# Optimization experiments

Hardware: AMD Instinct MI355X
Metric: run time of the kernel (lower is better)

The kernel has to match this reference:

```python
import jax, jax.numpy as jnp
import numpy as np

NEG_INF = -1e30  # stand-in for float('-inf') masked_fill (safe for softmax)


def setup_inputs() -> dict:
    key = jax.random.key(0)
    ks = jax.random.split(key, 7)
    B, T, C, H, D = 4, 2048, 64, 6, 64
    s = 1.0 / np.sqrt(C)
    return {
        "x": jax.random.normal(ks[0], (B, T, C), dtype=jnp.float32),
        "y": jax.random.normal(ks[1], (B, T, C), dtype=jnp.float32),
        "Wq": jax.random.normal(ks[2], (H, C, D), dtype=jnp.float32) * s,
        "Wk": jax.random.normal(ks[3], (H, C, D), dtype=jnp.float32) * s,
        "Wv": jax.random.normal(ks[4], (H, C, D), dtype=jnp.float32) * s,
        "W_proj": jax.random.normal(ks[5], (H * D, C), dtype=jnp.float32) * (1.0 / np.sqrt(H * D)),
        "b_proj": jnp.zeros((C,), dtype=jnp.float32),
    }


def reference(x, y, Wq, Wk, Wv, W_proj, b_proj):
    # x, y: [B, T, C]; per-head projections stacked over H (heads vectorized).
    B, T, C = x.shape
    H, _, D = Wq.shape
    q = jnp.einsum("btc,hcd->bhtd", x, Wq)   # query from decoder input x
    k = jnp.einsum("btc,hcd->bhtd", y, Wk)   # key from encoder output y
    v = jnp.einsum("btc,hcd->bhtd", y, Wv)
    scale = D ** (-0.5)
    wei = jnp.einsum("bhtd,bhsd->bhts", q, k) * scale  # [B,H,T,T]
    # triu(ones(T,T), diagonal=1) future mask (causal)
    future = jnp.triu(jnp.ones((T, T), dtype=bool), k=1)
    wei = jnp.where(future, NEG_INF, wei)
    wei = jax.nn.softmax(wei, axis=-1)  # dropout = identity in eval
    out = jnp.einsum("bhts,bhsd->bhtd", wei, v)          # [B,H,T,D]
    out = out.transpose(0, 2, 1, 3).reshape(B, T, H * D)  # concat heads
    return out @ W_proj + b_proj                          # [B,T,C]
```

## Files before the change

### kernel.cpp

```cpp
#include <hip/hip_runtime.h>


typedef unsigned short u16t;
typedef __attribute__((ext_vector_type(8))) short short8;
typedef __attribute__((ext_vector_type(4))) float float4v;

#define MFMA16(a, b, c) __builtin_amdgcn_mfma_f32_16x16x32_bf16((a), (b), (c), 0, 0, 0)

__device__ __forceinline__ float fexp2(float x) {
  return __builtin_amdgcn_exp2f(x);
}
__device__ __forceinline__ float bf2f(u16t u) {
  return __uint_as_float(((unsigned)u) << 16);
}
__device__ __forceinline__ u16t f2bf(float f) {
  unsigned u = __float_as_uint(f);
  u += 0x7fffu + ((u >> 16) & 1u);
  return (u16t)(u >> 16);
}
__device__ __forceinline__ u16t f2bf_trunc(float f) {
  return (u16t)(__float_as_uint(f) >> 16);
}
__device__ __forceinline__ short8 load8_f32_bf16(const float* p) {
  float4 f0 = *(const float4*)p;
  float4 f1 = *(const float4*)(p + 4);
  short8 r;
  r[0] = (short)f2bf(f0.x); r[1] = (short)f2bf(f0.y);
  r[2] = (short)f2bf(f0.z); r[3] = (short)f2bf(f0.w);
  r[4] = (short)f2bf(f1.x); r[5] = (short)f2bf(f1.y);
  r[6] = (short)f2bf(f1.z); r[7] = (short)f2bf(f1.w);
  return r;
}

constexpr int Bb = 4, Tt = 2048, Cc = 64, Hh = 6, Dd = 64;
constexpr int BH = Bb * Hh;
constexpr int NQT = Tt / 64;
constexpr int LDT = 72;
constexpr int LDV = 136;
#define QSCALE (0.125f * 1.44269504088896f)

__global__ __launch_bounds__(256) void qkv_kernel(
    const float* __restrict__ x, const float* __restrict__ y,
    const float* __restrict__ Wq, const float* __restrict__ Wk,
    const float* __restrict__ Wv,
    u16t* __restrict__ Q, u16t* __restrict__ K, u16t* __restrict__ Vt) {
  __shared__ __align__(16) u16t wtq[64 * LDT];
  __shared__ __align__(16) u16t wtk[64 * LDT];
  __shared__ __align__(16) u16t wtv[64 * LDT];

  int bid = blockIdx.x;
  int bh = bid >> 5, tt = bid & 31;
  int b = bh / Hh, h = bh - b * Hh;
  int tid = threadIdx.x;
  int w = tid >> 6, lane = tid & 63;
  int l15 = lane & 15, q4 = lane >> 4;

  {
    const float4* wq4 = (const float4*)(Wq + h * 4096);
    const float4* wk4 = (const float4*)(Wk + h * 4096);
    const float4* wv4 = (const float4*)(Wv + h * 4096);
#pragma unroll
    for (int i = 0; i < 4; ++i) {
      int fidx = tid + i * 256;
      float4 qv = wq4[fidx], kv = wk4[fidx], vv = wv4[fidx];
      int base = fidx * 4;
      int c = base >> 6, d0 = base & 63;
      wtq[(d0 + 0) * LDT + c] = f2bf(qv.x);
      wtq[(d0 + 1) * LDT + c] = f2bf(qv.y);
      wtq[(d0 + 2) * LDT + c] = f2bf(qv.z);
      wtq[(d0 + 3) * LDT + c] = f2bf(qv.w);
      wtk[(d0 + 0) * LDT + c] = f2bf(kv.x);
      wtk[(d0 + 1) * LDT + c] = f2bf(kv.y);
      wtk[(d0 + 2) * LDT + c] = f2bf(kv.z);
      wtk[(d0 + 3) * LDT + c] = f2bf(kv.w);
      wtv[(d0 + 0) * LDT + c] = f2bf(vv.x);
      wtv[(d0 + 1) * LDT + c] = f2bf(vv.y);
      wtv[(d0 + 2) * LDT + c] = f2bf(vv.z);
      wtv[(d0 + 3) * LDT + c] = f2bf(vv.w);
    }
  }

  int trow = tt * 64 + w * 16 + l15;
  const float* xrow = x + ((size_t)b * Tt + trow) * Cc;
  const float* yrow = y + ((size_t)b * Tt + trow) * Cc;
  short8 xa[2], ya[2];
#pragma unroll
  for (int kc = 0; kc < 2; ++kc) {
    xa[kc] = load8_f32_bf16(xrow + kc * 32 + q4 * 8);
    ya[kc] = load8_f32_bf16(yrow + kc * 32 + q4 * 8);
  }
  __syncthreads();

  float4v qa4[4], ka4[4], va4[4];
#pragma unroll
  for (int nc = 0; nc < 4; ++nc) {
    qa4[nc] = (float4v){0.f, 0.f, 0.f, 0.f};
    ka4[nc] = (float4v){0.f, 0.f, 0.f, 0.f};
    va4[nc] = (float4v){0.f, 0.f, 0.f, 0.f};
  }
#pragma unroll
  for (int nc = 0; nc < 4; ++nc) {
#pragma unroll
    for (int kc = 0; kc < 2; ++kc) {
      int off = (nc * 16 + l15) * LDT + kc * 32 + q4 * 8;
      short8 bq = *(const short8*)&wtq[off];
      short8 bk = *(const short8*)&wtk[off];
      short8 bv = *(const short8*)&wtv[off];
      qa4[nc] = MFMA16(xa[kc], bq, qa4[nc]);
      ka4[nc] = MFMA16(ya[kc], bk, ka4[nc]);
      va4[nc] = MFMA16(ya[kc], bv, va4[nc]);
    }
  }
  __syncthreads();

#pragma unroll
  for (int reg = 0; reg < 4; ++reg) {
    int rloc = w * 16 + q4 * 4 + reg;
#pragma unroll
    for (int nc = 0; nc < 4; ++nc) {
      wtq[rloc * LDT + nc * 16 + l15] = f2bf(qa4[nc][reg] * QSCALE);
      wtk[rloc * LDT + nc * 16 + l15] = f2bf(ka4[nc][reg]);
      wtv[(nc * 16 + l15) * LDT + rloc] = f2bf(va4[nc][reg]);
    }
  }
  __syncthreads();

  size_t tilebase = ((size_t)bh * Tt + tt * 64) * Dd;
#pragma unroll
  for (int i = 0; i < 2; ++i) {
    int id = tid * 2 + i;
    int row = id >> 3, c8 = id & 7;
    *(uint4*)&Q[tilebase + row * 64 + c8 * 8] = *(const uint4*)&wtq[row * LDT + c8 * 8];
    *(uint4*)&K[tilebase + row * 64 + c8 * 8] = *(const uint4*)&wtk[row * LDT + c8 * 8];
    *(uint4*)&Vt[((size_t)bh * 64 + row) * Tt + tt * 64 + c8 * 8] =
        *(const uint4*)&wtv[row * LDT + c8 * 8];
  }
}

__global__ __launch_bounds__(256) void attn_kernel(
    const u16t* __restrict__ Q, const u16t* __restrict__ K,
    const u16t* __restrict__ Vt, u16t* __restrict__ att) {
  __shared__ __align__(16) u16t Kl[128 * LDT];
  __shared__ __align__(16) u16t Vl[64 * LDV];
  __shared__ __align__(16) u16t Pl[4 * 16 * LDV];

  int bid = blockIdx.x;
  int bh = bid % BH;
  int qt = (NQT - 1) - bid / BH;
  int b = bh / Hh, h = bh - (bh / Hh) * Hh;
  int tid = threadIdx.x;
  int w = tid >> 6;
  int lane = tid & 63;
  int l15 = lane & 15, q4 = lane >> 4;

  const u16t* Qbase = Q + ((size_t)bh * Tt + qt * 64 + w * 16 + l15) * Dd;
  short8 qf0 = *(const short8*)(Qbase + q4 * 8);
  short8 qf1 = *(const short8*)(Qbase + 32 + q4 * 8);

  float4v O[4];
#pragma unroll
  for (int nc = 0; nc < 4; ++nc) O[nc] = (float4v){0.f, 0.f, 0.f, 0.f};
  float l_[4] = {0.f, 0.f, 0.f, 0.f};

  const u16t* Kbh = K + (size_t)bh * Tt * Dd;
  const u16t* Vbh = Vt + (size_t)bh * Dd * Tt;
  u16t* Pw = Pl + w * 16 * LDV;
  const int jmax = qt >> 1;

  for (int jt = 0; jt <= jmax; ++jt) {
    __syncthreads();
    {
      const u16t* ksrc = Kbh + (size_t)jt * 128 * 64;
      const u16t* vsrc = Vbh + jt * 128;
#pragma unroll
      for (int i = 0; i < 4; ++i) {
        int ci = tid + i * 256;
        int kr = ci >> 3, kc8 = ci & 7;
        *(uint4*)&Kl[kr * LDT + kc8 * 8] = *(const uint4*)(ksrc + kr * 64 + kc8 * 8);
        int vd = ci >> 4, vj8 = ci & 15;
        *(uint4*)&Vl[vd * LDV + vj8 * 8] = *(const uint4*)(vsrc + (size_t)vd * Tt + vj8 * 8);
      }
    }
    __syncthreads();

    float4v S[8];
#pragma unroll
    for (int nc = 0; nc < 8; ++nc) {
      short8 kf0 = *(const short8*)&Kl[(nc * 16 + l15) * LDT + q4 * 8];
      short8 kf1 = *(const short8*)&Kl[(nc * 16 + l15) * LDT + 32 + q4 * 8];
      float4v s = (float4v){0.f, 0.f, 0.f, 0.f};
      s = MFMA16(qf0, kf0, s);
      s = MFMA16(qf1, kf1, s);
      S[nc] = s;
    }

    if (jt == jmax) {
      int rloc = qt * 64 + w * 16 + q4 * 4;
      int cbase = jt * 128 + l15;
#pragma unroll
      for (int nc = 0; nc < 8; ++nc)
#pragma unroll
        for (int reg = 0; reg < 4; ++reg)
          if (cbase + nc * 16 > rloc + reg) S[nc][reg] = -1e30f;
    }

#pragma unroll
    for (int nc = 0; nc < 8; ++nc) {
#pragma unroll
      for (int reg = 0; reg < 4; ++reg) {
        float p = fexp2(S[nc][reg]);
        l_[reg] += p;
        Pw[(q4 * 4 + reg) * LDV + nc * 16 + l15] = f2bf_trunc(p);
      }
    }

    short8 pf[4];
#pragma unroll
    for (int kc2 = 0; kc2 < 4; ++kc2)
      pf[kc2] = *(const short8*)&Pw[l15 * LDV + kc2 * 32 + q4 * 8];
#pragma unroll
    for (int nc = 0; nc < 4; ++nc) {
#pragma unroll
      for (int kc2 = 0; kc2 < 4; ++kc2) {
        short8 vf = *(const short8*)&Vl[(nc * 16 + l15) * LDV + kc2 * 32 + q4 * 8];
        O[nc] = MFMA16(pf[kc2], vf, O[nc]);
      }
    }
  }

#pragma unroll
  for (int reg = 0; reg < 4; ++reg) {
    float s = l_[reg];
#pragma unroll
    for (int off = 1; off < 16; off <<= 1) s += __shfl_xor(s, off);
    float inv = 1.0f / s;
    int t = qt * 64 + w * 16 + q4 * 4 + reg;
    size_t obase = ((size_t)b * Tt + t) * (Hh * Dd) + h * Dd;
#pragma unroll
    for (int nc = 0; nc < 4; ++nc)
      att[obase + nc * 16 + l15] = f2bf(O[nc][reg] * inv);
  }
}

constexpr int LDP = 392;

__global__ __launch_bounds__(256) void proj_kernel(
    const u16t* __restrict__ att, const float* __restrict__ Wp,
    const float* __restrict__ bp, float* __restrict__ out) {
  __shared__ __align__(16) u16t wpt[64 * LDP];

  int bid = blockIdx.x;
  int tid = threadIdx.x;
  int w = tid >> 6, lane = tid & 63;
  int l15 = lane & 15, q4 = lane >> 4;

  const float4* wp4 = (const float4*)Wp;
#pragma unroll
  for (int i = 0; i < 24; ++i) {
    int fidx = tid + i * 256;
    float4 v = wp4[fidx];
    int base = fidx * 4;
    int r = base >> 6, c0 = base & 63;
    wpt[(c0 + 0) * LDP + r] = f2bf(v.x);
    wpt[(c0 + 1) * LDP + r] = f2bf(v.y);
    wpt[(c0 + 2) * LDP + r] = f2bf(v.z);
    wpt[(c0 + 3) * LDP + r] = f2bf(v.w);
  }
  __syncthreads();

  int row0 = bid * 64 + w * 16;
  const u16t* arow = att + (size_t)(row0 + l15) * 384;

  float4v acc[4];
#pragma unroll
  for (int nc = 0; nc < 4; ++nc) acc[nc] = (float4v){0.f, 0.f, 0.f, 0.f};

#pragma unroll
  for (int kc = 0; kc < 12; ++kc) {
    short8 a = *(const short8*)(arow + kc * 32 + q4 * 8);
#pragma unroll
    for (int nc = 0; nc < 4; ++nc) {
      short8 bfr = *(const short8*)&wpt[(nc * 16 + l15) * LDP + kc * 32 + q4 * 8];
      acc[nc] = MFMA16(a, bfr, acc[nc]);
    }
  }

  float bv[4];
#pragma unroll
  for (int nc = 0; nc < 4; ++nc) bv[nc] = bp[nc * 16 + l15];
#pragma unroll
  for (int reg = 0; reg < 4; ++reg) {
    int t = row0 + q4 * 4 + reg;
    size_t obase = (size_t)t * 64;
#pragma unroll
    for (int nc = 0; nc < 4; ++nc)
      out[obase + nc * 16 + l15] = acc[nc][reg] + bv[nc];
  }
}

extern "C" void kernel_launch(void* const* d_in, const int* in_sizes, int n_in,
                              void* d_out, int out_size, void* d_ws, size_t ws_size,
                              hipStream_t stream) {
  const float* x  = (const float*)d_in[0];
  const float* y  = (const float*)d_in[1];
  const float* Wq = (const float*)d_in[2];
  const float* Wk = (const float*)d_in[3];
  const float* Wv = (const float*)d_in[4];
  const float* Wp = (const float*)d_in[5];
  const float* bp = (const float*)d_in[6];
  float* out = (float*)d_out;

  const size_t NBH = (size_t)BH * Tt * Dd;
  u16t* Qs   = (u16t*)d_ws;
  u16t* Ks   = Qs + NBH;
  u16t* Vts  = Ks + NBH;
  u16t* attb = Vts + NBH;

  qkv_kernel<<<BH * NQT, 256, 0, stream>>>(x, y, Wq, Wk, Wv, Qs, Ks, Vts);
  attn_kernel<<<BH * NQT, 256, 0, stream>>>(Qs, Ks, Vts, attb);
  proj_kernel<<<(Bb * Tt) / 64, 256, 0, stream>>>(attb, Wp, bp, out);
}
```

Measured before the change: 122.5 us.

## Restructure attention to split key tiles across waves and reduce outputs in LDS

The attention kernel now gives each wave 16 keys of a 64-key tile for all 64 query rows, instead of one 16-row query slice against 128 keys. Scores are computed transposed so the probabilities feed the PV MFMA straight from registers, which removes the P round-trip through shared memory. The cost is that half of each 32-wide MFMA K dimension is zero-padded, and partial O and row sums must be reduced across waves through LDS. Shared memory shrinks and launch bounds request 3 blocks per CU to raise occupancy, while each thread now holds 16 accumulator vectors, which raises register pressure.

```diff
diff --git a/kernel.cpp b/kernel.cpp
--- a/kernel.cpp
+++ b/kernel.cpp
@@ -6,6 +6,8 @@
 typedef __attribute__((ext_vector_type(4))) float float4v;
 
 #define MFMA16(a, b, c) __builtin_amdgcn_mfma_f32_16x16x32_bf16((a), (b), (c), 0, 0, 0)
+
+union U8 { short8 s; unsigned u[4]; };
 
 __device__ __forceinline__ float fexp2(float x) {
   return __builtin_amdgcn_exp2f(x);
@@ -18,8 +20,8 @@
   u += 0x7fffu + ((u >> 16) & 1u);
   return (u16t)(u >> 16);
 }
-__device__ __forceinline__ u16t f2bf_trunc(float f) {
-  return (u16t)(__float_as_uint(f) >> 16);
+__device__ __forceinline__ unsigned bftr(float f) {
+  return __float_as_uint(f) >> 16;
 }
 __device__ __forceinline__ short8 load8_f32_bf16(const float* p) {
   float4 f0 = *(const float4*)p;
@@ -36,7 +38,7 @@
 constexpr int BH = Bb * Hh;
 constexpr int NQT = Tt / 64;
 constexpr int LDT = 72;
-constexpr int LDV = 136;
+constexpr int OST = 65;
 #define QSCALE (0.125f * 1.44269504088896f)
 
 __global__ __launch_bounds__(256) void qkv_kernel(
@@ -137,12 +139,14 @@
   }
 }
 
-__global__ __launch_bounds__(256) void attn_kernel(
+__global__ __launch_bounds__(256, 3) void attn_kernel(
     const u16t* __restrict__ Q, const u16t* __restrict__ K,
     const u16t* __restrict__ Vt, u16t* __restrict__ att) {
-  __shared__ __align__(16) u16t Kl[128 * LDT];
-  __shared__ __align__(16) u16t Vl[64 * LDV];
-  __shared__ __align__(16) u16t Pl[4 * 16 * LDV];
+  __shared__ __align__(16) unsigned char smem[64 * LDT * 2 * 2 + 256];
+  u16t* Kl = (u16t*)smem;
+  u16t* Vl = (u16t*)(smem + 64 * LDT * 2);
+  float* Ol = (float*)smem;
+  float* Ll = (float*)(smem + 64 * LDT * 2 * 2);
 
   int bid = blockIdx.x;
   int bh = bid % BH;
@@ -153,92 +157,110 @@
   int lane = tid & 63;
   int l15 = lane & 15, q4 = lane >> 4;
 
-  const u16t* Qbase = Q + ((size_t)bh * Tt + qt * 64 + w * 16 + l15) * Dd;
-  short8 qf0 = *(const short8*)(Qbase + q4 * 8);
-  short8 qf1 = *(const short8*)(Qbase + 32 + q4 * 8);
-
-  float4v O[4];
-#pragma unroll
-  for (int nc = 0; nc < 4; ++nc) O[nc] = (float4v){0.f, 0.f, 0.f, 0.f};
+  short8 qf[4][2];
+#pragma unroll
+  for (int it = 0; it < 4; ++it) {
+    const u16t* qb = Q + ((size_t)bh * Tt + qt * 64 + it * 16 + l15) * Dd;
+    qf[it][0] = *(const short8*)(qb + q4 * 8);
+    qf[it][1] = *(const short8*)(qb + 32 + q4 * 8);
+  }
+
+  float4v O[4][4];
+#pragma unroll
+  for (int it = 0; it < 4; ++it)
+#pragma unroll
+    for (int nc = 0; nc < 4; ++nc) O[it][nc] = (float4v){0.f, 0.f, 0.f, 0.f};
   float l_[4] = {0.f, 0.f, 0.f, 0.f};
 
   const u16t* Kbh = K + (size_t)bh * Tt * Dd;
   const u16t* Vbh = Vt + (size_t)bh * Dd * Tt;
-  u16t* Pw = Pl + w * 16 * LDV;
-  const int jmax = qt >> 1;
-
-  for (int jt = 0; jt <= jmax; ++jt) {
+
+  for (int jt = 0; jt <= qt; ++jt) {
     __syncthreads();
     {
-      const u16t* ksrc = Kbh + (size_t)jt * 128 * 64;
-      const u16t* vsrc = Vbh + jt * 128;
-#pragma unroll
-      for (int i = 0; i < 4; ++i) {
-        int ci = tid + i * 256;
-        int kr = ci >> 3, kc8 = ci & 7;
-        *(uint4*)&Kl[kr * LDT + kc8 * 8] = *(const uint4*)(ksrc + kr * 64 + kc8 * 8);
-        int vd = ci >> 4, vj8 = ci & 15;
-        *(uint4*)&Vl[vd * LDV + vj8 * 8] = *(const uint4*)(vsrc + (size_t)vd * Tt + vj8 * 8);
+      const u16t* ksrc = Kbh + (size_t)jt * 64 * 64;
+      const u16t* vsrc = Vbh + jt * 64;
+#pragma unroll
+      for (int i = 0; i < 2; ++i) {
+        int id = tid * 2 + i;
+        int r = id >> 3, c8 = id & 7;
+        *(uint4*)&Kl[r * LDT + c8 * 8] = *(const uint4*)(ksrc + r * 64 + c8 * 8);
+        *(uint4*)&Vl[r * LDT + c8 * 8] = *(const uint4*)(vsrc + (size_t)r * Tt + c8 * 8);
       }
     }
     __syncthreads();
 
-    float4v S[8];
-#pragma unroll
-    for (int nc = 0; nc < 8; ++nc) {
-      short8 kf0 = *(const short8*)&Kl[(nc * 16 + l15) * LDT + q4 * 8];
-      short8 kf1 = *(const short8*)&Kl[(nc * 16 + l15) * LDT + 32 + q4 * 8];
-      float4v s = (float4v){0.f, 0.f, 0.f, 0.f};
-      s = MFMA16(qf0, kf0, s);
-      s = MFMA16(qf1, kf1, s);
-      S[nc] = s;
-    }
-
-    if (jt == jmax) {
-      int rloc = qt * 64 + w * 16 + q4 * 4;
-      int cbase = jt * 128 + l15;
-#pragma unroll
-      for (int nc = 0; nc < 8; ++nc)
-#pragma unroll
-        for (int reg = 0; reg < 4; ++reg)
-          if (cbase + nc * 16 > rloc + reg) S[nc][reg] = -1e30f;
-    }
-
-#pragma unroll
-    for (int nc = 0; nc < 8; ++nc) {
+    short8 kf0 = *(const short8*)&Kl[(w * 16 + l15) * LDT + q4 * 8];
+    short8 kf1 = *(const short8*)&Kl[(w * 16 + l15) * LDT + 32 + q4 * 8];
+    short8 vf[4];
+#pragma unroll
+    for (int nc = 0; nc < 4; ++nc) {
+      uint2 vv = *(const uint2*)&Vl[(nc * 16 + l15) * LDT + w * 16 + q4 * 4];
+      U8 t;
+      t.u[0] = vv.x; t.u[1] = vv.y; t.u[2] = 0u; t.u[3] = 0u;
+      vf[nc] = t.s;
+    }
+
+    bool diag = (jt == qt);
+#pragma unroll
+    for (int it = 0; it < 4; ++it) {
+      if (diag && w > it) continue;
+      float4v S = (float4v){0.f, 0.f, 0.f, 0.f};
+      S = MFMA16(kf0, qf[it][0], S);
+      S = MFMA16(kf1, qf[it][1], S);
+      float p[4];
 #pragma unroll
       for (int reg = 0; reg < 4; ++reg) {
-        float p = fexp2(S[nc][reg]);
-        l_[reg] += p;
-        Pw[(q4 * 4 + reg) * LDV + nc * 16 + l15] = f2bf_trunc(p);
+        p[reg] = (diag && w == it && (q4 * 4 + reg) > l15) ? 0.f : fexp2(S[reg]);
+        l_[it] += p[reg];
       }
-    }
-
-    short8 pf[4];
-#pragma unroll
-    for (int kc2 = 0; kc2 < 4; ++kc2)
-      pf[kc2] = *(const short8*)&Pw[l15 * LDV + kc2 * 32 + q4 * 8];
-#pragma unroll
-    for (int nc = 0; nc < 4; ++nc) {
-#pragma unroll
-      for (int kc2 = 0; kc2 < 4; ++kc2) {
-        short8 vf = *(const short8*)&Vl[(nc * 16 + l15) * LDV + kc2 * 32 + q4 * 8];
-        O[nc] = MFMA16(pf[kc2], vf, O[nc]);
+      U8 pa;
+      pa.u[0] = bftr(p[0]) | (bftr(p[1]) << 16);
+      pa.u[1] = bftr(p[2]) | (bftr(p[3]) << 16);
+      pa.u[2] = 0u; pa.u[3] = 0u;
+#pragma unroll
+      for (int nc = 0; nc < 4; ++nc)
+        O[it][nc] = MFMA16(pa.s, vf[nc], O[it][nc]);
+    }
+  }
+
+#pragma unroll
+  for (int it = 0; it < 4; ++it) {
+    l_[it] += __shfl_xor(l_[it], 16);
+    l_[it] += __shfl_xor(l_[it], 32);
+  }
+
+  __syncthreads();
+#pragma unroll
+  for (int r = 0; r < 4; ++r) {
+    int it = (w + r) & 3;
+#pragma unroll
+    for (int nc = 0; nc < 4; ++nc)
+#pragma unroll
+      for (int reg = 0; reg < 4; ++reg) {
+        int addr = (it * 16 + q4 * 4 + reg) * OST + nc * 16 + l15;
+        if (r == 0) Ol[addr] = O[it][nc][reg];
+        else        Ol[addr] += O[it][nc][reg];
       }
-    }
-  }
-
-#pragma unroll
-  for (int reg = 0; reg < 4; ++reg) {
-    float s = l_[reg];
-#pragma unroll
-    for (int off = 1; off < 16; off <<= 1) s += __shfl_xor(s, off);
-    float inv = 1.0f / s;
-    int t = qt * 64 + w * 16 + q4 * 4 + reg;
-    size_t obase = ((size_t)b * Tt + t) * (Hh * Dd) + h * Dd;
-#pragma unroll
-    for (int nc = 0; nc < 4; ++nc)
-      att[obase + nc * 16 + l15] = f2bf(O[nc][reg] * inv);
+    if (q4 == 0) {
+      if (r == 0) Ll[it * 16 + l15] = l_[it];
+      else        Ll[it * 16 + l15] += l_[it];
+    }
+    __syncthreads();
+  }
+
+#pragma unroll
+  for (int i = 0; i < 2; ++i) {
+    int id = tid * 2 + i;
+    int row = id >> 3, c8 = id & 7;
+    float inv = 1.0f / Ll[row];
+    const float* orow = &Ol[row * OST + c8 * 8];
+    U8 o;
+#pragma unroll
+    for (int k = 0; k < 4; ++k)
+      o.u[k] = f2bf(orow[2 * k] * inv) | ((unsigned)f2bf(orow[2 * k + 1] * inv) << 16);
+    int t = qt * 64 + row;
+    *(uint4*)&att[((size_t)b * Tt + t) * (Hh * Dd) + h * Dd + c8 * 8] = *(const uint4*)&o;
   }
 }
 
```

Result: slower. 253.8 us (+107.2%).
